# Optimization experiments

Hardware: AMD Instinct MI355X
Metric: run time of the kernel (lower is better)

The kernel has to match this reference:

```python
import jax, jax.numpy as jnp
import numpy as np

DIM = 64  # per-head dim used for the sqrt scale


def setup_inputs() -> dict:
    key = jax.random.key(0)
    kq, kk, kv, ke, kf = jax.random.split(key, 5)
    B, N, d, k = 32, 4096, 64, 256
    Q = jax.random.normal(kq, (B, N, d), dtype=jnp.float32)
    K = jax.random.normal(kk, (B, N, d), dtype=jnp.float32)
    V = jax.random.normal(kv, (B, N, d), dtype=jnp.float32)
    E = jax.random.normal(ke, (N, k), dtype=jnp.float32) * (1.0 / np.sqrt(N))
    F = jax.random.normal(kf, (N, k), dtype=jnp.float32) * (1.0 / np.sqrt(N))
    return {"Q": Q, "K": K, "V": V, "E": E, "F": F}


def reference(Q, K, V, E, F):
    # Linformer head: K^T E -> [B,d,k]; Q (K^T E) / sqrt(d) -> [B,N,k]
    K_proj = jnp.einsum('bnd,nk->bdk', K, E)          # low-rank key projection
    scores = jnp.einsum('bnd,bdk->bnk', Q, K_proj) / jnp.sqrt(jnp.float32(DIM))
    P_bar = jax.nn.softmax(scores, axis=2)            # [B,N,k]
    # (V^T F)^T -> [B,k,d]
    V_proj = jnp.einsum('bnd,nk->bkd', V, F)
    return jnp.einsum('bnk,bkd->bnd', P_bar, V_proj)  # [B,N,d]
```

## Files before the change

### kernel.cpp

```cpp
#include <hip/hip_runtime.h>
#include <hip/hip_bf16.h>

#define BB 32
#define NN 4096
#define DDIM 64

typedef __attribute__((ext_vector_type(8)))  short bf16x8;
typedef __attribute__((ext_vector_type(16))) float f32x16;
typedef __attribute__((ext_vector_type(4)))  float f32x4;

static __device__ inline unsigned short f2bf(float x) {
  union { float f; unsigned u; } v; v.f = x;
  unsigned r = (v.u + 0x7FFFu + ((v.u >> 16) & 1u)) >> 16;
  return (unsigned short)r;
}

static __device__ inline unsigned pk(float a, float b) {
  union { __hip_bfloat162 h; unsigned u; } c;
  c.h = __float22bfloat162_rn(float2{a, b});
  return c.u;
}

static __device__ inline bf16x8 pack8(const float* f) {
  union { unsigned u[4]; bf16x8 v; } r;
  r.u[0] = pk(f[0], f[1]); r.u[1] = pk(f[2], f[3]);
  r.u[2] = pk(f[4], f[5]); r.u[3] = pk(f[6], f[7]);
  return r.v;
}

template <int SA, int SB, int OS>
static __device__ inline void proj_body(
    const float* __restrict__ As, const float* __restrict__ Bs,
    float* __restrict__ Cg, int mAdd, int nAdd, int chunk, int h, int lr)
{
  f32x16 acc[2][2];
#pragma unroll
  for (int i = 0; i < 2; ++i)
#pragma unroll
    for (int j = 0; j < 2; ++j)
#pragma unroll
      for (int q = 0; q < 16; ++q) acc[i][j][q] = 0.f;

  const int n0 = chunk * 1024 + h * 8;
  const float* pA = As + (long)n0 * SA + mAdd + lr;
  const float* pB = Bs + (long)n0 * SB + nAdd + lr;

#pragma unroll 2
  for (int tt = 0; tt < 64; ++tt) {
    const float* qA = pA + (long)tt * 16 * SA;
    const float* qB = pB + (long)tt * 16 * SB;
    float a0[8], a1[8], b0[8], b1[8];
#pragma unroll
    for (int j = 0; j < 8; ++j) {
      a0[j] = qA[j * SA];      a1[j] = qA[j * SA + 32];
      b0[j] = qB[j * SB];      b1[j] = qB[j * SB + 32];
    }
    bf16x8 A0 = pack8(a0), A1 = pack8(a1);
    bf16x8 B0 = pack8(b0), B1 = pack8(b1);
    acc[0][0] = __builtin_amdgcn_mfma_f32_32x32x16_bf16(A0, B0, acc[0][0], 0, 0, 0);
    acc[0][1] = __builtin_amdgcn_mfma_f32_32x32x16_bf16(A0, B1, acc[0][1], 0, 0, 0);
    acc[1][0] = __builtin_amdgcn_mfma_f32_32x32x16_bf16(A1, B0, acc[1][0], 0, 0, 0);
    acc[1][1] = __builtin_amdgcn_mfma_f32_32x32x16_bf16(A1, B1, acc[1][1], 0, 0, 0);
  }

#pragma unroll
  for (int mt = 0; mt < 2; ++mt)
#pragma unroll
    for (int nt = 0; nt < 2; ++nt)
#pragma unroll
      for (int i = 0; i < 16; ++i) {
        int ro  = (i & 3) + 8 * (i >> 2) + 4 * h;
        int row = mAdd + mt * 32 + ro;
        int col = nAdd + nt * 32 + lr;
        Cg[row * OS + col] = acc[mt][nt][i];
      }
}

__global__ __launch_bounds__(256) void proj_gemm(
    const float* __restrict__ Kg, const float* __restrict__ Vg,
    const float* __restrict__ Eg, const float* __restrict__ Fg,
    float* __restrict__ KpP, float* __restrict__ VpP)
{
  const int blk = blockIdx.x;
  const int chunk = blk & 3, mat = (blk >> 2) & 1, b = blk >> 3;
  const int t = threadIdx.x, w = t >> 6, l = t & 63, h = l >> 5, lr = l & 31;

  if (mat == 0) {
    proj_body<256, 64, 64>(Eg, Kg + (long)b * NN * DDIM,
                           KpP + (long)chunk * (BB * 16384) + b * 16384,
                           w * 64, 0, chunk, h, lr);
  } else {
    proj_body<64, 256, 256>(Vg + (long)b * NN * DDIM, Fg,
                            VpP + (long)chunk * (BB * 16384) + b * 16384,
                            0, w * 64, chunk, h, lr);
  }
}

__global__ __launch_bounds__(256) void reduce_cvt(
    const float* __restrict__ KpP, const float* __restrict__ VpP,
    unsigned short* __restrict__ Kpb, unsigned short* __restrict__ Vpb)
{
  const int blk = blockIdx.x;
  const float* src = (blk < 256) ? KpP : VpP;
  unsigned short* dst = (blk < 256) ? Kpb : Vpb;
  const long i = (long)(blk & 255) * 2048 + threadIdx.x * 8;
  float a[8];
#pragma unroll
  for (int j = 0; j < 8; ++j) a[j] = 0.f;
#pragma unroll
  for (int cch = 0; cch < 4; ++cch) {
    const float4 p0 = *(const float4*)(src + (long)cch * (BB * 16384) + i);
    const float4 p1 = *(const float4*)(src + (long)cch * (BB * 16384) + i + 4);
    a[0] += p0.x; a[1] += p0.y; a[2] += p0.z; a[3] += p0.w;
    a[4] += p1.x; a[5] += p1.y; a[6] += p1.z; a[7] += p1.w;
  }
  unsigned short o[8];
#pragma unroll
  for (int j = 0; j < 8; ++j) o[j] = f2bf(a[j]);
  *(bf16x8*)(dst + i) = *(const bf16x8*)&o[0];
}

__global__ __launch_bounds__(256, 2) void attn2_kernel(
    const float* __restrict__ Qg, const unsigned short* __restrict__ Kpb,
    const unsigned short* __restrict__ Vpb, float* __restrict__ Og)
{
  extern __shared__ float O_lds[];

  const int blk = blockIdx.x;
  const int b = blk >> 4, rg = blk & 15;
  const int t = threadIdx.x, w = t >> 6, l = t & 63;
  const int h = l >> 5, lr = l & 31;
  const int rbase = rg * 256 + w * 64;

  const unsigned short* Kp = Kpb + (long)b * 16384;
  const unsigned short* Vp = Vpb + (long)b * 16384;

  bf16x8 Bq[2][4];
#pragma unroll
  for (int rt = 0; rt < 2; ++rt)
#pragma unroll
    for (int kk = 0; kk < 4; ++kk) {
      const float* qp = Qg + ((long)b * NN + rbase + rt * 32 + lr) * 64 + kk * 16 + h * 8;
      float4 x = *(const float4*)qp;
      float4 y = *(const float4*)(qp + 4);
      union { unsigned u[4]; bf16x8 v; } r;
      r.u[0] = pk(x.x, x.y); r.u[1] = pk(x.z, x.w);
      r.u[2] = pk(y.x, y.y); r.u[3] = pk(y.z, y.w);
      Bq[rt][kk] = r.v;
    }

  f32x16 o[2][2];
#pragma unroll
  for (int rt = 0; rt < 2; ++rt)
#pragma unroll
    for (int dt = 0; dt < 2; ++dt)
#pragma unroll
      for (int q = 0; q < 16; ++q) o[rt][dt][q] = 0.f;
  float rowpart[2] = {0.f, 0.f};

  union UV { uint4 u; bf16x8 v; };

#pragma unroll
  for (int kt = 0; kt < 8; ++kt) {
    bf16x8 Ak[4];
#pragma unroll
    for (int kk = 0; kk < 4; ++kk)
      Ak[kk] = *(const bf16x8*)(Kp + (long)(kt * 32 + lr) * 64 + kk * 16 + h * 8);
    bf16x8 Av[2][2];
#pragma unroll
    for (int dt = 0; dt < 2; ++dt)
#pragma unroll
      for (int kc = 0; kc < 2; ++kc)
        Av[dt][kc] = *(const bf16x8*)(Vp + (long)(dt * 32 + lr) * 256 + (kt * 2 + kc) * 16 + h * 8);

#pragma unroll
    for (int rt = 0; rt < 2; ++rt) {
      f32x16 s;
#pragma unroll
      for (int q = 0; q < 16; ++q) s[q] = 0.f;
#pragma unroll
      for (int kk = 0; kk < 4; ++kk)
        s = __builtin_amdgcn_mfma_f32_32x32x16_bf16(Ak[kk], Bq[rt][kk], s, 0, 0, 0);

      float p[16];
#pragma unroll
      for (int q = 0; q < 16; ++q) p[q] = exp2f(s[q] * 0.1803368801f);
      rowpart[rt] += (((p[0] + p[1]) + (p[2] + p[3])) + ((p[4] + p[5]) + (p[6] + p[7])))
                   + (((p[8] + p[9]) + (p[10] + p[11])) + ((p[12] + p[13]) + (p[14] + p[15])));

      unsigned wv[8];
#pragma unroll
      for (int m = 0; m < 8; ++m) wv[m] = pk(p[2 * m], p[2 * m + 1]);
      unsigned r02 = __shfl_xor(h ? wv[0] : wv[2], 32);
      unsigned r13 = __shfl_xor(h ? wv[1] : wv[3], 32);
      unsigned r46 = __shfl_xor(h ? wv[4] : wv[6], 32);
      unsigned r57 = __shfl_xor(h ? wv[5] : wv[7], 32);
      UV c0, c1;
      if (h == 0) {
        c0.u = uint4{wv[0], wv[1], r02, r13};
        c1.u = uint4{wv[4], wv[5], r46, r57};
      } else {
        c0.u = uint4{r02, r13, wv[2], wv[3]};
        c1.u = uint4{r46, r57, wv[6], wv[7]};
      }
      o[rt][0] = __builtin_amdgcn_mfma_f32_32x32x16_bf16(Av[0][0], c0.v, o[rt][0], 0, 0, 0);
      o[rt][0] = __builtin_amdgcn_mfma_f32_32x32x16_bf16(Av[0][1], c1.v, o[rt][0], 0, 0, 0);
      o[rt][1] = __builtin_amdgcn_mfma_f32_32x32x16_bf16(Av[1][0], c0.v, o[rt][1], 0, 0, 0);
      o[rt][1] = __builtin_amdgcn_mfma_f32_32x32x16_bf16(Av[1][1], c1.v, o[rt][1], 0, 0, 0);
    }
  }

#pragma unroll
  for (int rt = 0; rt < 2; ++rt) {
    float rowsum = rowpart[rt] + __shfl_xor(rowpart[rt], 32);
    float inv = __builtin_amdgcn_rcpf(rowsum);
    const int r = w * 64 + rt * 32 + lr;
#pragma unroll
    for (int dt = 0; dt < 2; ++dt)
#pragma unroll
      for (int qg = 0; qg < 4; ++qg) {
        f32x4 vq;
        vq[0] = o[rt][dt][qg * 4 + 0] * inv;
        vq[1] = o[rt][dt][qg * 4 + 1] * inv;
        vq[2] = o[rt][dt][qg * 4 + 2] * inv;
        vq[3] = o[rt][dt][qg * 4 + 3] * inv;
        int cd = dt * 8 + 2 * qg + h;
        int cp = cd ^ (r & 15);
        *(f32x4*)&O_lds[r * 64 + cp * 4] = vq;
      }
  }
  __syncthreads();

  const long obase = ((long)b * NN + rg * 256) * 64;
#pragma unroll
  for (int i = 0; i < 16; ++i) {
    int ci = i * 256 + t;
    int rr = ci >> 4, cc = ci & 15, cp = cc ^ (rr & 15);
    *(float4*)(Og + obase + rr * 64 + cc * 4) = *(const float4*)&O_lds[rr * 64 + cp * 4];
  }
}

extern "C" void kernel_launch(void* const* d_in, const int* in_sizes, int n_in,
                              void* d_out, int out_size, void* d_ws, size_t ws_size,
                              hipStream_t stream) {
  const float* Q = (const float*)d_in[0];
  const float* K = (const float*)d_in[1];
  const float* V = (const float*)d_in[2];
  const float* E = (const float*)d_in[3];
  const float* F = (const float*)d_in[4];
  float* out = (float*)d_out;

  char* ws = (char*)d_ws;
  float*          KpP = (float*)(ws);
  float*          VpP = (float*)(ws + (8l << 20));
  unsigned short* Kpb = (unsigned short*)(ws + (16l << 20));
  unsigned short* Vpb = (unsigned short*)(ws + (17l << 20));

  proj_gemm<<<dim3(256), dim3(256), 0, stream>>>(K, V, E, F, KpP, VpP);

  reduce_cvt<<<dim3(512), dim3(256), 0, stream>>>(KpP, VpP, Kpb, Vpb);

  hipFuncSetAttribute((const void*)attn2_kernel,
                      hipFuncAttributeMaxDynamicSharedMemorySize, 65536);
  attn2_kernel<<<dim3(512), dim3(256), 65536, stream>>>(Q, Kpb, Vpb, out);
}
```

Before: 202.4 us.

## Split projection GEMM into more N-chunks and double-buffer its global loads

The projection GEMM now splits the N reduction into 8 chunks instead of 4, which doubles the grid to 512 blocks, and sets launch_bounds occupancy to 2. The inner loop is also rewritten into a manual two-stage register double buffer, so the next tile's global loads are issued before the current MFMAs. The point is to fill more CUs and hide load latency in a kernel bound by memory latency. The cost is twice the partial-sum workspace, more traffic in the reduce step, and more register pressure. The 4-chunk path stays as a fallback when the workspace is too small.

```diff
diff --git a/kernel.cpp b/kernel.cpp
--- a/kernel.cpp
+++ b/kernel.cpp
@@ -28,11 +28,40 @@
   return r.v;
 }
 
-template <int SA, int SB, int OS>
+template <int SA, int SB>
+static __device__ inline void load_set(
+    const float* __restrict__ pA, const float* __restrict__ pB, int t,
+    float a0[8], float a1[8], float b0[8], float b1[8])
+{
+  const float* qA = pA + (long)t * 16 * SA;
+  const float* qB = pB + (long)t * 16 * SB;
+#pragma unroll
+  for (int j = 0; j < 8; ++j) {
+    a0[j] = qA[j * SA];      a1[j] = qA[j * SA + 32];
+    b0[j] = qB[j * SB];      b1[j] = qB[j * SB + 32];
+  }
+}
+
+static __device__ inline void mfma4(
+    f32x16 acc[2][2],
+    const float a0[8], const float a1[8], const float b0[8], const float b1[8])
+{
+  bf16x8 A0 = pack8(a0), A1 = pack8(a1);
+  bf16x8 B0 = pack8(b0), B1 = pack8(b1);
+  acc[0][0] = __builtin_amdgcn_mfma_f32_32x32x16_bf16(A0, B0, acc[0][0], 0, 0, 0);
+  acc[0][1] = __builtin_amdgcn_mfma_f32_32x32x16_bf16(A0, B1, acc[0][1], 0, 0, 0);
+  acc[1][0] = __builtin_amdgcn_mfma_f32_32x32x16_bf16(A1, B0, acc[1][0], 0, 0, 0);
+  acc[1][1] = __builtin_amdgcn_mfma_f32_32x32x16_bf16(A1, B1, acc[1][1], 0, 0, 0);
+}
+
+template <int SA, int SB, int OS, int NCH>
 static __device__ inline void proj_body(
     const float* __restrict__ As, const float* __restrict__ Bs,
     float* __restrict__ Cg, int mAdd, int nAdd, int chunk, int h, int lr)
 {
+  constexpr int CN = NN / NCH;
+  constexpr int T  = CN / 16;
+
   f32x16 acc[2][2];
 #pragma unroll
   for (int i = 0; i < 2; ++i)
@@ -41,26 +70,21 @@
 #pragma unroll
       for (int q = 0; q < 16; ++q) acc[i][j][q] = 0.f;
 
-  const int n0 = chunk * 1024 + h * 8;
+  const int n0 = chunk * CN + h * 8;
   const float* pA = As + (long)n0 * SA + mAdd + lr;
   const float* pB = Bs + (long)n0 * SB + nAdd + lr;
 
-#pragma unroll 2
-  for (int tt = 0; tt < 64; ++tt) {
-    const float* qA = pA + (long)tt * 16 * SA;
-    const float* qB = pB + (long)tt * 16 * SB;
-    float a0[8], a1[8], b0[8], b1[8];
-#pragma unroll
-    for (int j = 0; j < 8; ++j) {
-      a0[j] = qA[j * SA];      a1[j] = qA[j * SA + 32];
-      b0[j] = qB[j * SB];      b1[j] = qB[j * SB + 32];
-    }
-    bf16x8 A0 = pack8(a0), A1 = pack8(a1);
-    bf16x8 B0 = pack8(b0), B1 = pack8(b1);
-    acc[0][0] = __builtin_amdgcn_mfma_f32_32x32x16_bf16(A0, B0, acc[0][0], 0, 0, 0);
-    acc[0][1] = __builtin_amdgcn_mfma_f32_32x32x16_bf16(A0, B1, acc[0][1], 0, 0, 0);
-    acc[1][0] = __builtin_amdgcn_mfma_f32_32x32x16_bf16(A1, B0, acc[1][0], 0, 0, 0);
-    acc[1][1] = __builtin_amdgcn_mfma_f32_32x32x16_bf16(A1, B1, acc[1][1], 0, 0, 0);
+  float xa0[8], xa1[8], xb0[8], xb1[8];
+  float ya0[8], ya1[8], yb0[8], yb1[8];
+
+  load_set<SA, SB>(pA, pB, 0, xa0, xa1, xb0, xb1);
+
+  for (int tt = 0; tt < T; tt += 2) {
+    load_set<SA, SB>(pA, pB, tt + 1, ya0, ya1, yb0, yb1);
+    mfma4(acc, xa0, xa1, xb0, xb1);
+    const int tn = (tt + 2 < T) ? (tt + 2) : 0;
+    load_set<SA, SB>(pA, pB, tn, xa0, xa1, xb0, xb1);
+    mfma4(acc, ya0, ya1, yb0, yb1);
   }
 
 #pragma unroll
@@ -76,26 +100,30 @@
       }
 }
 
-__global__ __launch_bounds__(256) void proj_gemm(
+template <int NCH>
+__global__ __launch_bounds__(256, 2) void proj_gemm(
     const float* __restrict__ Kg, const float* __restrict__ Vg,
     const float* __restrict__ Eg, const float* __restrict__ Fg,
     float* __restrict__ KpP, float* __restrict__ VpP)
 {
   const int blk = blockIdx.x;
-  const int chunk = blk & 3, mat = (blk >> 2) & 1, b = blk >> 3;
+  const int chunk = blk % NCH;
+  const int mat = (blk / NCH) & 1, b = blk / (2 * NCH);
   const int t = threadIdx.x, w = t >> 6, l = t & 63, h = l >> 5, lr = l & 31;
+  const long PSTR = (long)BB * 16384;
 
   if (mat == 0) {
-    proj_body<256, 64, 64>(Eg, Kg + (long)b * NN * DDIM,
-                           KpP + (long)chunk * (BB * 16384) + b * 16384,
-                           w * 64, 0, chunk, h, lr);
+    proj_body<256, 64, 64, NCH>(Eg, Kg + (long)b * NN * DDIM,
+                                KpP + (long)chunk * PSTR + b * 16384,
+                                w * 64, 0, chunk, h, lr);
   } else {
-    proj_body<64, 256, 256>(Vg + (long)b * NN * DDIM, Fg,
-                            VpP + (long)chunk * (BB * 16384) + b * 16384,
-                            0, w * 64, chunk, h, lr);
-  }
-}
-
+    proj_body<64, 256, 256, NCH>(Vg + (long)b * NN * DDIM, Fg,
+                                 VpP + (long)chunk * PSTR + b * 16384,
+                                 0, w * 64, chunk, h, lr);
+  }
+}
+
+template <int NCH>
 __global__ __launch_bounds__(256) void reduce_cvt(
     const float* __restrict__ KpP, const float* __restrict__ VpP,
     unsigned short* __restrict__ Kpb, unsigned short* __restrict__ Vpb)
@@ -108,7 +136,7 @@
 #pragma unroll
   for (int j = 0; j < 8; ++j) a[j] = 0.f;
 #pragma unroll
-  for (int cch = 0; cch < 4; ++cch) {
+  for (int cch = 0; cch < NCH; ++cch) {
     const float4 p0 = *(const float4*)(src + (long)cch * (BB * 16384) + i);
     const float4 p1 = *(const float4*)(src + (long)cch * (BB * 16384) + i + 4);
     a[0] += p0.x; a[1] += p0.y; a[2] += p0.z; a[3] += p0.w;
@@ -251,16 +279,28 @@
   float* out = (float*)d_out;
 
   char* ws = (char*)d_ws;
-  float*          KpP = (float*)(ws);
-  float*          VpP = (float*)(ws + (8l << 20));
-  unsigned short* Kpb = (unsigned short*)(ws + (16l << 20));
-  unsigned short* Vpb = (unsigned short*)(ws + (17l << 20));
-
-  proj_gemm<<<dim3(256), dim3(256), 0, stream>>>(K, V, E, F, KpP, VpP);
-
-  reduce_cvt<<<dim3(512), dim3(256), 0, stream>>>(KpP, VpP, Kpb, Vpb);
+  const long SLAB = (long)BB * 16384 * 4;
 
   hipFuncSetAttribute((const void*)attn2_kernel,
                       hipFuncAttributeMaxDynamicSharedMemorySize, 65536);
-  attn2_kernel<<<dim3(512), dim3(256), 65536, stream>>>(Q, Kpb, Vpb, out);
-}
+
+  if (ws_size >= (size_t)(16 * SLAB + (2l << 20))) {
+    float*          KpP = (float*)(ws);
+    float*          VpP = (float*)(ws + 8 * SLAB);
+    unsigned short* Kpb = (unsigned short*)(ws + 16 * SLAB);
+    unsigned short* Vpb = Kpb + 524288;
+
+    proj_gemm<8><<<dim3(512), dim3(256), 0, stream>>>(K, V, E, F, KpP, VpP);
+    reduce_cvt<8><<<dim3(512), dim3(256), 0, stream>>>(KpP, VpP, Kpb, Vpb);
+    attn2_kernel<<<dim3(512), dim3(256), 65536, stream>>>(Q, Kpb, Vpb, out);
+  } else {
+    float*          KpP = (float*)(ws);
+    float*          VpP = (float*)(ws + 4 * SLAB);
+    unsigned short* Kpb = (unsigned short*)(ws + 8 * SLAB);
+    unsigned short* Vpb = Kpb + 524288;
+
+    proj_gemm<4><<<dim3(256), dim3(256), 0, stream>>>(K, V, E, F, KpP, VpP);
+    reduce_cvt<4><<<dim3(512), dim3(256), 0, stream>>>(KpP, VpP, Kpb, Vpb);
+    attn2_kernel<<<dim3(512), dim3(256), 65536, stream>>>(Q, Kpb, Vpb, out);
+  }
+}
```

Result: faster. 190.8 us (-5.7%).

## Pre-pack K/V/E/F to bf16 fragment layout, split projection wider, stage Kp/Vp in LDS

Applied to the files above, without the earlier changes.

Adds a prep kernel that converts E, F, K and V to bf16 in an MFMA-fragment-friendly interleaved layout. The projection GEMM can then issue vector loads instead of strided scalar fp32 loads with on-the-fly packing. The reduction over N is split into 8 chunks instead of 4 for more blocks, and the reduce kernel sums 8 partials. The attention kernel copies the per-batch Kp/Vp into swizzled LDS once rather than reading global memory per tile. The cost is an extra kernel launch and an extra full pass writing and reading bf16 copies of K and V.

```diff
diff --git a/kernel.cpp b/kernel.cpp
--- a/kernel.cpp
+++ b/kernel.cpp
@@ -4,6 +4,7 @@
 #define BB 32
 #define NN 4096
 #define DDIM 64
+#define NCH 8
 
 typedef __attribute__((ext_vector_type(8)))  short bf16x8;
 typedef __attribute__((ext_vector_type(16))) float f32x16;
@@ -21,17 +22,49 @@
   return c.u;
 }
 
-static __device__ inline bf16x8 pack8(const float* f) {
-  union { unsigned u[4]; bf16x8 v; } r;
-  r.u[0] = pk(f[0], f[1]); r.u[1] = pk(f[2], f[3]);
-  r.u[2] = pk(f[4], f[5]); r.u[3] = pk(f[6], f[7]);
-  return r.v;
-}
-
-template <int SA, int SB, int OS>
-static __device__ inline void proj_body(
-    const float* __restrict__ As, const float* __restrict__ Bs,
-    float* __restrict__ Cg, int mAdd, int nAdd, int chunk, int h, int lr)
+__global__ __launch_bounds__(256) void prep_frag(
+    const float* __restrict__ Eg, const float* __restrict__ Fg,
+    const float* __restrict__ Kg, const float* __restrict__ Vg,
+    unsigned short* __restrict__ Ebt, unsigned short* __restrict__ Fbt,
+    unsigned short* __restrict__ Kbt, unsigned short* __restrict__ Vbt)
+{
+  const int blk = blockIdx.x, t = threadIdx.x;
+  float v[8];
+  if (blk < 1024) {
+    const int which = blk >> 9;
+    const int nbg = blk & 511;
+    const float* src = (which ? Fg : Eg) + (long)(nbg * 8) * 256 + t;
+    unsigned short* dst = (which ? Fbt : Ebt) + ((long)nbg * 256 + t) * 8;
+#pragma unroll
+    for (int j = 0; j < 8; ++j) v[j] = src[j * 256];
+    union { unsigned u[4]; bf16x8 x; } r;
+    r.u[0] = pk(v[0], v[1]); r.u[1] = pk(v[2], v[3]);
+    r.u[2] = pk(v[4], v[5]); r.u[3] = pk(v[6], v[7]);
+    *(bf16x8*)dst = r.x;
+  } else {
+    const int kb = blk - 1024;
+    const int which = kb >> 12;
+    const int kb2 = kb & 4095;
+    const int b = kb2 >> 7, nb = kb2 & 127;
+    const int g = t >> 6, d = t & 63;
+    const int nbg = nb * 4 + g;
+    const float* src = (which ? Vg : Kg) + ((long)b * NN + nbg * 8) * 64 + d;
+    unsigned short* dst = (which ? Vbt : Kbt)
+                        + (long)b * 262144 + ((long)nbg * 64 + d) * 8;
+#pragma unroll
+    for (int j = 0; j < 8; ++j) v[j] = src[j * 64];
+    union { unsigned u[4]; bf16x8 x; } r;
+    r.u[0] = pk(v[0], v[1]); r.u[1] = pk(v[2], v[3]);
+    r.u[2] = pk(v[4], v[5]); r.u[3] = pk(v[6], v[7]);
+    *(bf16x8*)dst = r.x;
+  }
+}
+
+template <int MAT>
+static __device__ inline void proj_core5(
+    const unsigned short* __restrict__ Bigt,
+    const unsigned short* __restrict__ Smlt,
+    float* __restrict__ Cg, int w, int h, int lr, int chunk)
 {
   f32x16 acc[2][2];
 #pragma unroll
@@ -41,28 +74,48 @@
 #pragma unroll
       for (int q = 0; q < 16; ++q) acc[i][j][q] = 0.f;
 
-  const int n0 = chunk * 1024 + h * 8;
-  const float* pA = As + (long)n0 * SA + mAdd + lr;
-  const float* pB = Bs + (long)n0 * SB + nAdd + lr;
-
-#pragma unroll 2
-  for (int tt = 0; tt < 64; ++tt) {
-    const float* qA = pA + (long)tt * 16 * SA;
-    const float* qB = pB + (long)tt * 16 * SB;
-    float a0[8], a1[8], b0[8], b1[8];
-#pragma unroll
-    for (int j = 0; j < 8; ++j) {
-      a0[j] = qA[j * SA];      a1[j] = qA[j * SA + 32];
-      b0[j] = qB[j * SB];      b1[j] = qB[j * SB + 32];
-    }
-    bf16x8 A0 = pack8(a0), A1 = pack8(a1);
-    bf16x8 B0 = pack8(b0), B1 = pack8(b1);
-    acc[0][0] = __builtin_amdgcn_mfma_f32_32x32x16_bf16(A0, B0, acc[0][0], 0, 0, 0);
-    acc[0][1] = __builtin_amdgcn_mfma_f32_32x32x16_bf16(A0, B1, acc[0][1], 0, 0, 0);
-    acc[1][0] = __builtin_amdgcn_mfma_f32_32x32x16_bf16(A1, B0, acc[1][0], 0, 0, 0);
-    acc[1][1] = __builtin_amdgcn_mfma_f32_32x32x16_bf16(A1, B1, acc[1][1], 0, 0, 0);
-  }
-
+  const int colB = w * 64 + lr;
+  const unsigned short* pB0 = Bigt + (((long)chunk * 16 * 4 + h) * 256 + colB) * 8;
+  const unsigned short* pB1 = pB0 + 2 * 256 * 8;
+  const unsigned short* pS0 = Smlt + (((long)chunk * 16 * 4 + h) * 64 + lr) * 8;
+  const unsigned short* pS1 = pS0 + 2 * 64 * 8;
+
+#pragma unroll 4
+  for (int tt = 0; tt < 16; ++tt) {
+    const long ob = (long)tt * (1024 * 8);
+    const long os = (long)tt * (256 * 8);
+    bf16x8 B0a = *(const bf16x8*)(pB0 + ob);
+    bf16x8 B0b = *(const bf16x8*)(pB0 + ob + 32 * 8);
+    bf16x8 B1a = *(const bf16x8*)(pB1 + ob);
+    bf16x8 B1b = *(const bf16x8*)(pB1 + ob + 32 * 8);
+    bf16x8 S0a = *(const bf16x8*)(pS0 + os);
+    bf16x8 S0b = *(const bf16x8*)(pS0 + os + 32 * 8);
+    bf16x8 S1a = *(const bf16x8*)(pS1 + os);
+    bf16x8 S1b = *(const bf16x8*)(pS1 + os + 32 * 8);
+    if (MAT == 0) {
+      acc[0][0] = __builtin_amdgcn_mfma_f32_32x32x16_bf16(B0a, S0a, acc[0][0], 0, 0, 0);
+      acc[0][1] = __builtin_amdgcn_mfma_f32_32x32x16_bf16(B0a, S0b, acc[0][1], 0, 0, 0);
+      acc[1][0] = __builtin_amdgcn_mfma_f32_32x32x16_bf16(B0b, S0a, acc[1][0], 0, 0, 0);
+      acc[1][1] = __builtin_amdgcn_mfma_f32_32x32x16_bf16(B0b, S0b, acc[1][1], 0, 0, 0);
+      acc[0][0] = __builtin_amdgcn_mfma_f32_32x32x16_bf16(B1a, S1a, acc[0][0], 0, 0, 0);
+      acc[0][1] = __builtin_amdgcn_mfma_f32_32x32x16_bf16(B1a, S1b, acc[0][1], 0, 0, 0);
+      acc[1][0] = __builtin_amdgcn_mfma_f32_32x32x16_bf16(B1b, S1a, acc[1][0], 0, 0, 0);
+      acc[1][1] = __builtin_amdgcn_mfma_f32_32x32x16_bf16(B1b, S1b, acc[1][1], 0, 0, 0);
+    } else {
+      acc[0][0] = __builtin_amdgcn_mfma_f32_32x32x16_bf16(S0a, B0a, acc[0][0], 0, 0, 0);
+      acc[0][1] = __builtin_amdgcn_mfma_f32_32x32x16_bf16(S0a, B0b, acc[0][1], 0, 0, 0);
+      acc[1][0] = __builtin_amdgcn_mfma_f32_32x32x16_bf16(S0b, B0a, acc[1][0], 0, 0, 0);
+      acc[1][1] = __builtin_amdgcn_mfma_f32_32x32x16_bf16(S0b, B0b, acc[1][1], 0, 0, 0);
+      acc[0][0] = __builtin_amdgcn_mfma_f32_32x32x16_bf16(S1a, B1a, acc[0][0], 0, 0, 0);
+      acc[0][1] = __builtin_amdgcn_mfma_f32_32x32x16_bf16(S1a, B1b, acc[0][1], 0, 0, 0);
+      acc[1][0] = __builtin_amdgcn_mfma_f32_32x32x16_bf16(S1b, B1a, acc[1][0], 0, 0, 0);
+      acc[1][1] = __builtin_amdgcn_mfma_f32_32x32x16_bf16(S1b, B1b, acc[1][1], 0, 0, 0);
+    }
+  }
+
+  const int mAdd = (MAT == 0) ? w * 64 : 0;
+  const int nAdd = (MAT == 0) ? 0 : w * 64;
+  const int OS   = (MAT == 0) ? 64 : 256;
 #pragma unroll
   for (int mt = 0; mt < 2; ++mt)
 #pragma unroll
@@ -76,23 +129,23 @@
       }
 }
 
-__global__ __launch_bounds__(256) void proj_gemm(
-    const float* __restrict__ Kg, const float* __restrict__ Vg,
-    const float* __restrict__ Eg, const float* __restrict__ Fg,
+__global__ __launch_bounds__(256, 2) void proj_gemm(
+    const unsigned short* __restrict__ Ebt, const unsigned short* __restrict__ Fbt,
+    const unsigned short* __restrict__ Kbt, const unsigned short* __restrict__ Vbt,
     float* __restrict__ KpP, float* __restrict__ VpP)
 {
   const int blk = blockIdx.x;
-  const int chunk = blk & 3, mat = (blk >> 2) & 1, b = blk >> 3;
+  const int chunk = blk % NCH;
+  const int mat = (blk / NCH) & 1, b = blk / (2 * NCH);
   const int t = threadIdx.x, w = t >> 6, l = t & 63, h = l >> 5, lr = l & 31;
+  const long PSTR = (long)BB * 16384;
 
   if (mat == 0) {
-    proj_body<256, 64, 64>(Eg, Kg + (long)b * NN * DDIM,
-                           KpP + (long)chunk * (BB * 16384) + b * 16384,
-                           w * 64, 0, chunk, h, lr);
+    proj_core5<0>(Ebt, Kbt + (long)b * 262144,
+                  KpP + (long)chunk * PSTR + b * 16384, w, h, lr, chunk);
   } else {
-    proj_body<64, 256, 256>(Vg + (long)b * NN * DDIM, Fg,
-                            VpP + (long)chunk * (BB * 16384) + b * 16384,
-                            0, w * 64, chunk, h, lr);
+    proj_core5<1>(Fbt, Vbt + (long)b * 262144,
+                  VpP + (long)chunk * PSTR + b * 16384, w, h, lr, chunk);
   }
 }
 
@@ -108,7 +161,7 @@
 #pragma unroll
   for (int j = 0; j < 8; ++j) a[j] = 0.f;
 #pragma unroll
-  for (int cch = 0; cch < 4; ++cch) {
+  for (int cch = 0; cch < NCH; ++cch) {
     const float4 p0 = *(const float4*)(src + (long)cch * (BB * 16384) + i);
     const float4 p1 = *(const float4*)(src + (long)cch * (BB * 16384) + i + 4);
     a[0] += p0.x; a[1] += p0.y; a[2] += p0.z; a[3] += p0.w;
@@ -124,16 +177,13 @@
     const float* __restrict__ Qg, const unsigned short* __restrict__ Kpb,
     const unsigned short* __restrict__ Vpb, float* __restrict__ Og)
 {
-  extern __shared__ float O_lds[];
+  extern __shared__ char smem[];
 
   const int blk = blockIdx.x;
   const int b = blk >> 4, rg = blk & 15;
   const int t = threadIdx.x, w = t >> 6, l = t & 63;
   const int h = l >> 5, lr = l & 31;
   const int rbase = rg * 256 + w * 64;
-
-  const unsigned short* Kp = Kpb + (long)b * 16384;
-  const unsigned short* Vp = Vpb + (long)b * 16384;
 
   bf16x8 Bq[2][4];
 #pragma unroll
@@ -149,6 +199,22 @@
       Bq[rt][kk] = r.v;
     }
 
+  {
+    const uint4* gk = (const uint4*)(Kpb + (long)b * 16384);
+    const uint4* gv = (const uint4*)(Vpb + (long)b * 16384);
+#pragma unroll
+    for (int i = 0; i < 8; ++i) {
+      int u = i * 256 + t;
+      uint4 x = gk[u];
+      int kbyte = (u * 16) ^ (((u >> 3) & 7) << 4);
+      *(uint4*)(smem + kbyte) = x;
+      uint4 y = gv[u];
+      int vbyte = (u * 16) ^ (((u >> 5) & 7) << 4);
+      *(uint4*)(smem + 32768 + vbyte) = y;
+    }
+  }
+  __syncthreads();
+
   f32x16 o[2][2];
 #pragma unroll
   for (int rt = 0; rt < 2; ++rt)
@@ -159,19 +225,24 @@
   float rowpart[2] = {0.f, 0.f};
 
   union UV { uint4 u; bf16x8 v; };
+  const int swz = (lr & 7) << 4;
 
 #pragma unroll
   for (int kt = 0; kt < 8; ++kt) {
     bf16x8 Ak[4];
 #pragma unroll
-    for (int kk = 0; kk < 4; ++kk)
-      Ak[kk] = *(const bf16x8*)(Kp + (long)(kt * 32 + lr) * 64 + kk * 16 + h * 8);
+    for (int kk = 0; kk < 4; ++kk) {
+      int byte = (kt * 32 + lr) * 128 + kk * 32 + h * 16;
+      Ak[kk] = *(const bf16x8*)(smem + (byte ^ swz));
+    }
     bf16x8 Av[2][2];
 #pragma unroll
     for (int dt = 0; dt < 2; ++dt)
 #pragma unroll
-      for (int kc = 0; kc < 2; ++kc)
-        Av[dt][kc] = *(const bf16x8*)(Vp + (long)(dt * 32 + lr) * 256 + (kt * 2 + kc) * 16 + h * 8);
+      for (int kc = 0; kc < 2; ++kc) {
+        int byte = (dt * 32 + lr) * 512 + (kt * 2 + kc) * 32 + h * 16;
+        Av[dt][kc] = *(const bf16x8*)(smem + 32768 + (byte ^ swz));
+      }
 
 #pragma unroll
     for (int rt = 0; rt < 2; ++rt) {
@@ -210,6 +281,9 @@
     }
   }
 
+  __syncthreads();
+  float* O_lds = (float*)smem;
+
 #pragma unroll
   for (int rt = 0; rt < 2; ++rt) {
     float rowsum = rowpart[rt] + __shfl_xor(rowpart[rt], 32);
@@ -252,15 +326,22 @@
 
   char* ws = (char*)d_ws;
   float*          KpP = (float*)(ws);
-  float*          VpP = (float*)(ws + (8l << 20));
-  unsigned short* Kpb = (unsigned short*)(ws + (16l << 20));
-  unsigned short* Vpb = (unsigned short*)(ws + (17l << 20));
-
-  proj_gemm<<<dim3(256), dim3(256), 0, stream>>>(K, V, E, F, KpP, VpP);
-
-  reduce_cvt<<<dim3(512), dim3(256), 0, stream>>>(KpP, VpP, Kpb, Vpb);
+  float*          VpP = (float*)(ws + (16l << 20));
+  unsigned short* Kpb = (unsigned short*)(ws + (32l << 20));
+  unsigned short* Vpb = (unsigned short*)(ws + (33l << 20));
+  unsigned short* Ebt = (unsigned short*)(ws + (34l << 20));
+  unsigned short* Fbt = (unsigned short*)(ws + (36l << 20));
+  unsigned short* Kbt = (unsigned short*)(ws + (38l << 20));
+  unsigned short* Vbt = (unsigned short*)(ws + (54l << 20));
 
   hipFuncSetAttribute((const void*)attn2_kernel,
                       hipFuncAttributeMaxDynamicSharedMemorySize, 65536);
+
+  prep_frag<<<dim3(9216), dim3(256), 0, stream>>>(E, F, K, V, Ebt, Fbt, Kbt, Vbt);
+
+  proj_gemm<<<dim3(512), dim3(256), 0, stream>>>(Ebt, Fbt, Kbt, Vbt, KpP, VpP);
+
+  reduce_cvt<<<dim3(512), dim3(256), 0, stream>>>(KpP, VpP, Kpb, Vpb);
+
   attn2_kernel<<<dim3(512), dim3(256), 65536, stream>>>(Q, Kpb, Vpb, out);
 }
```

Measured after the change: 193.1 us. 4.6% less time.

## Stage projection GEMM through LDS with async triple-buffered loads and more chunks

Applied to the files above, without the earlier changes.

The projection GEMM now copies E/F and K/V tiles into LDS with global_load_lds DMA, triple-buffered and gated by explicit vmcnt waits and barriers, instead of strided per-lane global loads. The N dimension is split into 8 chunks instead of 4, doubling the grid to 512 blocks for better CU occupancy, and the reduce kernel sums 8 partials. The intent is to coalesce the strided global reads and overlap memory with MFMA work. In exchange it writes and reads twice as much fp32 partial data in the reduction, and the hand-placed waitcnt sequencing is fragile.

```diff
diff --git a/kernel.cpp b/kernel.cpp
--- a/kernel.cpp
+++ b/kernel.cpp
@@ -4,16 +4,11 @@
 #define BB 32
 #define NN 4096
 #define DDIM 64
+#define NCH 8
 
 typedef __attribute__((ext_vector_type(8)))  short bf16x8;
 typedef __attribute__((ext_vector_type(16))) float f32x16;
 typedef __attribute__((ext_vector_type(4)))  float f32x4;
-
-static __device__ inline unsigned short f2bf(float x) {
-  union { float f; unsigned u; } v; v.f = x;
-  unsigned r = (v.u + 0x7FFFu + ((v.u >> 16) & 1u)) >> 16;
-  return (unsigned short)r;
-}
 
 static __device__ inline unsigned pk(float a, float b) {
   union { __hip_bfloat162 h; unsigned u; } c;
@@ -28,11 +23,24 @@
   return r.v;
 }
 
-template <int SA, int SB, int OS>
-static __device__ inline void proj_body(
-    const float* __restrict__ As, const float* __restrict__ Bs,
-    float* __restrict__ Cg, int mAdd, int nAdd, int chunk, int h, int lr)
+static __device__ __forceinline__ void dma16(const float* g, float* l) {
+  __builtin_amdgcn_global_load_lds(
+      (const __attribute__((address_space(1))) void*)g,
+      (__attribute__((address_space(3))) void*)l, 16, 0, 0);
+}
+
+template <int MAT>
+static __device__ inline void proj_core7(
+    const float* __restrict__ Gbig,
+    const float* __restrict__ Gsml,
+    float* __restrict__ Cg,
+    float (*Bs)[4096], float (*Ss)[1024], int chunk)
 {
+  const int t = threadIdx.x, w = t >> 6, l = t & 63, h = l >> 5, lr = l & 31;
+
+  const float* pbB = Gbig + (long)(chunk * 512) * 256;
+  const float* pbS = Gsml + (long)(chunk * 512) * 64;
+
   f32x16 acc[2][2];
 #pragma unroll
   for (int i = 0; i < 2; ++i)
@@ -41,28 +49,60 @@
 #pragma unroll
       for (int q = 0; q < 16; ++q) acc[i][j][q] = 0.f;
 
-  const int n0 = chunk * 1024 + h * 8;
-  const float* pA = As + (long)n0 * SA + mAdd + lr;
-  const float* pB = Bs + (long)n0 * SB + nAdd + lr;
-
-#pragma unroll 2
-  for (int tt = 0; tt < 64; ++tt) {
-    const float* qA = pA + (long)tt * 16 * SA;
-    const float* qB = pB + (long)tt * 16 * SB;
-    float a0[8], a1[8], b0[8], b1[8];
+  auto issue = [&](int step, int buf) {
+    const float* gb = pbB + (long)step * (16 * 256) + w * 1024 + l * 4;
+    float* lb = &Bs[buf][w * 1024];
+#pragma unroll
+    for (int i = 0; i < 4; ++i)
+      dma16(gb + i * 256, lb + i * 256);
+    dma16(pbS + (long)step * (16 * 64) + w * 256 + l * 4, &Ss[buf][w * 256]);
+  };
+
+  auto consume = [&](int buf) {
+    float fB0[8], fB1[8], fS0[8], fS1[8];
 #pragma unroll
     for (int j = 0; j < 8; ++j) {
-      a0[j] = qA[j * SA];      a1[j] = qA[j * SA + 32];
-      b0[j] = qB[j * SB];      b1[j] = qB[j * SB + 32];
-    }
-    bf16x8 A0 = pack8(a0), A1 = pack8(a1);
-    bf16x8 B0 = pack8(b0), B1 = pack8(b1);
-    acc[0][0] = __builtin_amdgcn_mfma_f32_32x32x16_bf16(A0, B0, acc[0][0], 0, 0, 0);
-    acc[0][1] = __builtin_amdgcn_mfma_f32_32x32x16_bf16(A0, B1, acc[0][1], 0, 0, 0);
-    acc[1][0] = __builtin_amdgcn_mfma_f32_32x32x16_bf16(A1, B0, acc[1][0], 0, 0, 0);
-    acc[1][1] = __builtin_amdgcn_mfma_f32_32x32x16_bf16(A1, B1, acc[1][1], 0, 0, 0);
-  }
-
+      const int rB = (h * 8 + j) * 256 + w * 64 + lr;
+      const int rS = (h * 8 + j) * 64 + lr;
+      fB0[j] = Bs[buf][rB];  fB1[j] = Bs[buf][rB + 32];
+      fS0[j] = Ss[buf][rS];  fS1[j] = Ss[buf][rS + 32];
+    }
+    bf16x8 B0 = pack8(fB0), B1 = pack8(fB1);
+    bf16x8 S0 = pack8(fS0), S1 = pack8(fS1);
+    if (MAT == 0) {
+      acc[0][0] = __builtin_amdgcn_mfma_f32_32x32x16_bf16(B0, S0, acc[0][0], 0, 0, 0);
+      acc[0][1] = __builtin_amdgcn_mfma_f32_32x32x16_bf16(B0, S1, acc[0][1], 0, 0, 0);
+      acc[1][0] = __builtin_amdgcn_mfma_f32_32x32x16_bf16(B1, S0, acc[1][0], 0, 0, 0);
+      acc[1][1] = __builtin_amdgcn_mfma_f32_32x32x16_bf16(B1, S1, acc[1][1], 0, 0, 0);
+    } else {
+      acc[0][0] = __builtin_amdgcn_mfma_f32_32x32x16_bf16(S0, B0, acc[0][0], 0, 0, 0);
+      acc[0][1] = __builtin_amdgcn_mfma_f32_32x32x16_bf16(S0, B1, acc[0][1], 0, 0, 0);
+      acc[1][0] = __builtin_amdgcn_mfma_f32_32x32x16_bf16(S1, B0, acc[1][0], 0, 0, 0);
+      acc[1][1] = __builtin_amdgcn_mfma_f32_32x32x16_bf16(S1, B1, acc[1][1], 0, 0, 0);
+    }
+  };
+
+  issue(0, 0);
+  issue(1, 1);
+
+  int buf = 0;
+#pragma unroll 1
+  for (int tt = 0; tt < 32; ++tt) {
+    if (tt < 31) asm volatile("s_waitcnt vmcnt(5)" ::: "memory");
+    else         asm volatile("s_waitcnt vmcnt(0)" ::: "memory");
+    __builtin_amdgcn_s_barrier();
+    __builtin_amdgcn_sched_barrier(0);
+    consume(buf);
+    if (tt + 2 < 32) {
+      int nb = buf + 2; if (nb >= 3) nb -= 3;
+      issue(tt + 2, nb);
+    }
+    buf = (buf == 2) ? 0 : buf + 1;
+  }
+
+  const int mAdd = (MAT == 0) ? w * 64 : 0;
+  const int nAdd = (MAT == 0) ? 0 : w * 64;
+  const int OS   = (MAT == 0) ? 64 : 256;
 #pragma unroll
   for (int mt = 0; mt < 2; ++mt)
 #pragma unroll
@@ -76,23 +116,25 @@
       }
 }
 
-__global__ __launch_bounds__(256) void proj_gemm(
+__global__ __launch_bounds__(256, 2) void proj_gemm(
     const float* __restrict__ Kg, const float* __restrict__ Vg,
     const float* __restrict__ Eg, const float* __restrict__ Fg,
     float* __restrict__ KpP, float* __restrict__ VpP)
 {
+  __shared__ float Bs[3][4096];
+  __shared__ float Ss[3][1024];
+
   const int blk = blockIdx.x;
-  const int chunk = blk & 3, mat = (blk >> 2) & 1, b = blk >> 3;
-  const int t = threadIdx.x, w = t >> 6, l = t & 63, h = l >> 5, lr = l & 31;
+  const int chunk = blk % NCH;
+  const int mat = (blk / NCH) & 1, b = blk / (2 * NCH);
+  const long PSTR = (long)BB * 16384;
 
   if (mat == 0) {
-    proj_body<256, 64, 64>(Eg, Kg + (long)b * NN * DDIM,
-                           KpP + (long)chunk * (BB * 16384) + b * 16384,
-                           w * 64, 0, chunk, h, lr);
+    proj_core7<0>(Eg, Kg + (long)b * NN * DDIM,
+                  KpP + (long)chunk * PSTR + b * 16384, Bs, Ss, chunk);
   } else {
-    proj_body<64, 256, 256>(Vg + (long)b * NN * DDIM, Fg,
-                            VpP + (long)chunk * (BB * 16384) + b * 16384,
-                            0, w * 64, chunk, h, lr);
+    proj_core7<1>(Fg, Vg + (long)b * NN * DDIM,
+                  VpP + (long)chunk * PSTR + b * 16384, Bs, Ss, chunk);
   }
 }
 
@@ -101,23 +143,18 @@
     unsigned short* __restrict__ Kpb, unsigned short* __restrict__ Vpb)
 {
   const int blk = blockIdx.x;
-  const float* src = (blk < 256) ? KpP : VpP;
-  unsigned short* dst = (blk < 256) ? Kpb : Vpb;
-  const long i = (long)(blk & 255) * 2048 + threadIdx.x * 8;
-  float a[8];
-#pragma unroll
-  for (int j = 0; j < 8; ++j) a[j] = 0.f;
-#pragma unroll
-  for (int cch = 0; cch < 4; ++cch) {
-    const float4 p0 = *(const float4*)(src + (long)cch * (BB * 16384) + i);
-    const float4 p1 = *(const float4*)(src + (long)cch * (BB * 16384) + i + 4);
-    a[0] += p0.x; a[1] += p0.y; a[2] += p0.z; a[3] += p0.w;
-    a[4] += p1.x; a[5] += p1.y; a[6] += p1.z; a[7] += p1.w;
-  }
-  unsigned short o[8];
-#pragma unroll
-  for (int j = 0; j < 8; ++j) o[j] = f2bf(a[j]);
-  *(bf16x8*)(dst + i) = *(const bf16x8*)&o[0];
+  const float* src = (blk < 512) ? KpP : VpP;
+  unsigned short* dst = (blk < 512) ? Kpb : Vpb;
+  const long i = (long)(blk & 511) * 1024 + threadIdx.x * 4;
+  float a0 = 0.f, a1 = 0.f, a2 = 0.f, a3 = 0.f;
+#pragma unroll
+  for (int cch = 0; cch < NCH; ++cch) {
+    const float4 p = *(const float4*)(src + (long)cch * (BB * 16384) + i);
+    a0 += p.x; a1 += p.y; a2 += p.z; a3 += p.w;
+  }
+  uint2 o;
+  o.x = pk(a0, a1); o.y = pk(a2, a3);
+  *(uint2*)(dst + i) = o;
 }
 
 __global__ __launch_bounds__(256, 2) void attn2_kernel(
@@ -252,15 +289,16 @@
 
   char* ws = (char*)d_ws;
   float*          KpP = (float*)(ws);
-  float*          VpP = (float*)(ws + (8l << 20));
-  unsigned short* Kpb = (unsigned short*)(ws + (16l << 20));
-  unsigned short* Vpb = (unsigned short*)(ws + (17l << 20));
-
-  proj_gemm<<<dim3(256), dim3(256), 0, stream>>>(K, V, E, F, KpP, VpP);
-
-  reduce_cvt<<<dim3(512), dim3(256), 0, stream>>>(KpP, VpP, Kpb, Vpb);
+  float*          VpP = (float*)(ws + (16l << 20));
+  unsigned short* Kpb = (unsigned short*)(ws + (32l << 20));
+  unsigned short* Vpb = (unsigned short*)(ws + (33l << 20));
 
   hipFuncSetAttribute((const void*)attn2_kernel,
                       hipFuncAttributeMaxDynamicSharedMemorySize, 65536);
+
+  proj_gemm<<<dim3(512), dim3(256), 0, stream>>>(K, V, E, F, KpP, VpP);
+
+  reduce_cvt<<<dim3(1024), dim3(256), 0, stream>>>(KpP, VpP, Kpb, Vpb);
+
   attn2_kernel<<<dim3(512), dim3(256), 65536, stream>>>(Q, Kpb, Vpb, out);
 }
```

New measurement: 192.9 us. 1.05x faster.
